# Optimization experiments

Measured on AMD Instinct MI355X. Metric: run time of the kernel, lower is better.

## Reference

```python
import jax, jax.numpy as jnp
import numpy as np
import math

B, T, IN, H, OUT, L = 8, 256, 128, 128, 128, 2
MAX_EP_LEN = 10000.0


def _rotate(x, pos, d):
    # rope as in source: repeat(1,1,2) = concat along last dim (not interleave)
    half = jnp.exp(jnp.arange(0, d, 2, dtype=jnp.float32) * (-math.log(MAX_EP_LEN) / d))  # [d/2]
    ang = pos[..., None] * half  # [B,T,d/2]
    sine = jnp.concatenate([jnp.sin(ang), jnp.sin(ang)], axis=-1)
    cos = jnp.concatenate([jnp.cos(ang), jnp.cos(ang)], axis=-1)
    y1, y2 = jnp.split(x, 2, axis=-1)
    x_rot = jnp.concatenate([-y2, y1], axis=-1)
    return x * cos + x_rot * sine


def _layernorm(x, w, b, eps=1e-5):
    m = jnp.mean(x, axis=-1, keepdims=True)
    v = jnp.mean((x - m) ** 2, axis=-1, keepdims=True)
    return (x - m) / jnp.sqrt(v + eps) * w + b


def _block(x, S0, Z0, Wk, Wq, Wv, lw, lb, w1, b1, w2, b2, scw, scb):
    # x: [B,T,F]; S0: [B,F,F]; Z0: [B,F]
    x = _layernorm(x, lw, lb)
    K = jax.nn.elu(x @ Wk.T) + 1.0
    Q = jax.nn.elu(x @ Wq.T) + 1.0
    V = x @ Wv.T
    outer = jnp.einsum('bti,btj->btij', K, V)  # [B,T,F,F]
    S = jnp.clip(jnp.cumsum(outer, axis=1), -1e20, 1e20) + S0[:, None]  # [B,T,F,F]
    Z = jnp.clip(jnp.cumsum(K, axis=1), -1e20, 1e20) + Z0[:, None]      # [B,T,F]
    num = jnp.einsum('bti,btil->btl', Q, S)
    den = jnp.einsum('bti,bti->bt', Q, Z)[..., None] + 1e-5
    out = num / den
    out = jax.nn.relu(jax.nn.relu(out @ w1.T + b1) @ w2.T + b2)  # feed_forward
    out = out + x @ scw.T + scb                                   # residual shortcut
    return out, S[:, -1], Z[:, -1]


def setup_inputs() -> dict:
    key = jax.random.key(0)
    ks = jax.random.split(key, 14)
    s = 0.05
    return {
        'z': jax.random.normal(ks[0], (T, B, IN), jnp.float32),
        'state': jnp.zeros((B, L * (H * H + H) + 1), jnp.float32),
        'Wk': jax.random.normal(ks[1], (L, H, IN), jnp.float32) * s,
        'Wq': jax.random.normal(ks[2], (L, H, IN), jnp.float32) * s,
        'Wv': jax.random.normal(ks[3], (L, H, IN), jnp.float32) * s,
        'ln_w': jnp.ones((L, IN), jnp.float32),
        'ln_b': jnp.zeros((L, IN), jnp.float32),
        'ff_w1': jax.random.normal(ks[4], (L, H, H), jnp.float32) * s,
        'ff_b1': jnp.zeros((L, H), jnp.float32),
        'ff_w2': jax.random.normal(ks[5], (L, H, H), jnp.float32) * s,
        'ff_b2': jnp.zeros((L, H), jnp.float32),
        'sc_w': jax.random.normal(ks[6], (L, H, IN), jnp.float32) * s,
        'sc_b': jnp.zeros((L, H), jnp.float32),
        'unmap_w': jax.random.normal(ks[7], (OUT, H), jnp.float32) * s,
        'unmap_b': jnp.zeros((OUT,), jnp.float32),
    }


def reference(z, state, Wk, Wq, Wv, ln_w, ln_b, ff_w1, ff_b1, ff_w2, ff_b2, sc_w, sc_b, unmap_w, unmap_b):
    x = jnp.transpose(z, (1, 0, 2))  # [B,T,IN]
    ts = state[:, -1]                # [B] timestep counters
    core = state[:, :-1].reshape(B, L, H * H + H)
    pos = ts[:, None] + jnp.arange(T, dtype=jnp.float32)[None, :]  # [B,T]
    x = _rotate(x, pos, IN)  # embedding_type == 'rope'
    new_states = []
    for i in range(L):
        S0 = core[:, i, :H * H].reshape(B, H, H)
        Z0 = core[:, i, H * H:]
        x, Sl, Zl = _block(x, S0, Z0, Wk[i], Wq[i], Wv[i], ln_w[i], ln_b[i],
                           ff_w1[i], ff_b1[i], ff_w2[i], ff_b2[i], sc_w[i], sc_b[i])
        new_states.append(jnp.concatenate([Sl.reshape(B, -1), Zl], axis=-1))
    y = x @ unmap_w.T + unmap_b
    st = jnp.concatenate([jnp.stack(new_states, axis=1).reshape(B, -1), (ts + T)[:, None]], axis=-1)
    return jnp.transpose(y, (1, 0, 2)), st
```

## Files before the change

kernel.cpp:

```cpp
#include <hip/hip_runtime.h>
#include <math.h>

#define Bn 8
#define Tn 256
#define Hn 128
#define Ln 2
#define COREn (Hn*Hn + Hn)
#define SDn   (Ln*COREn + 1)

typedef __attribute__((ext_vector_type(8))) short short8;
typedef __attribute__((ext_vector_type(4))) short short4v;
typedef __attribute__((ext_vector_type(4))) float floatx4;

#define MFMA16(a,b,c) __builtin_amdgcn_mfma_f32_16x16x32_bf16(a,b,c,0,0,0)

static __device__ __forceinline__ unsigned short f2bf(float f) {
  unsigned int u = __float_as_uint(f);
  return (unsigned short)((u + 0x7FFFu + ((u >> 16) & 1u)) >> 16);
}
static __device__ __forceinline__ float bf2f(unsigned short h) {
  return __uint_as_float((unsigned int)h << 16);
}
static __device__ __forceinline__ short8 ldwfrag(const float* p) {
  float4 a = *(const float4*)p;
  float4 b = *(const float4*)(p + 4);
  short8 r;
  r[0] = (short)f2bf(a.x); r[1] = (short)f2bf(a.y);
  r[2] = (short)f2bf(a.z); r[3] = (short)f2bf(a.w);
  r[4] = (short)f2bf(b.x); r[5] = (short)f2bf(b.y);
  r[6] = (short)f2bf(b.z); r[7] = (short)f2bf(b.w);
  return r;
}
static __device__ __forceinline__ void ld8(const float* p, float* v) {
  float4 a = *(const float4*)p, b = *(const float4*)(p + 4);
  v[0]=a.x; v[1]=a.y; v[2]=a.z; v[3]=a.w; v[4]=b.x; v[5]=b.y; v[6]=b.z; v[7]=b.w;
}

__global__ __launch_bounds__(256) void proj_kernel(
    const float* __restrict__ xsrc, const float* __restrict__ state,
    const float* __restrict__ Wk, const float* __restrict__ Wq,
    const float* __restrict__ Wv, const float* __restrict__ scw,
    const float* __restrict__ lnw, const float* __restrict__ lnb,
    const float* __restrict__ scb,
    unsigned short* __restrict__ Kb, unsigned short* __restrict__ Kt,
    unsigned short* __restrict__ Qb, unsigned short* __restrict__ Vt,
    float* __restrict__ skipb, int is_l0) {
  __shared__ unsigned short xs[16][136];

  const int tid = threadIdx.x;
  const int by  = blockIdx.y;
  const int g0  = blockIdx.x * 16;
  const int r = tid >> 4, c0 = (tid & 15) * 8;
  const int g = g0 + r, b = g >> 8, t = g & 255;

  float v[8];
  if (is_l0) {
    const float* zr = xsrc + ((size_t)t * Bn + b) * 128;
    float pv[8];
    ld8(zr + c0, v);
    ld8(zr + (c0 ^ 64), pv);
    float pos = state[(size_t)b * SDn + SDn - 1] + (float)t;
#pragma unroll
    for (int i = 0; i < 8; i++) {
      int jj = (c0 + i) & 63;
      float ang = pos * expf((float)jj * -0.14391156831212787f);
      float sn = sinf(ang), cs = cosf(ang);
      v[i] = (c0 < 64) ? (v[i] * cs - pv[i] * sn) : (v[i] * cs + pv[i] * sn);
    }
  } else {
    ld8(xsrc + (size_t)g * 128 + c0, v);
  }
  float sm = 0.f, sq = 0.f;
#pragma unroll
  for (int i = 0; i < 8; i++) { sm += v[i]; sq += v[i] * v[i]; }
  for (int d = 8; d; d >>= 1) { sm += __shfl_xor(sm, d, 16); sq += __shfl_xor(sq, d, 16); }
  float mean = sm * (1.f / 128.f);
  float rstd = rsqrtf(sq * (1.f / 128.f) - mean * mean + 1e-5f);
  float lw[8], lb[8];
  ld8(lnw + c0, lw); ld8(lnb + c0, lb);
  short8 xv;
#pragma unroll
  for (int i = 0; i < 8; i++) xv[i] = (short)f2bf((v[i] - mean) * rstd * lw[i] + lb[i]);
  *(short8*)&xs[r][c0] = xv;
  __syncthreads();

  const float* Wsel = (by == 0) ? Wk : (by == 1) ? Wq : (by == 2) ? Wv : scw;
  const int lane = tid & 63, wv = tid >> 6;
  const int lm = lane & 15, quad = lane >> 4;
  floatx4 acc0 = {0.f, 0.f, 0.f, 0.f}, acc1 = {0.f, 0.f, 0.f, 0.f};
#pragma unroll
  for (int kc = 0; kc < 4; kc++) {
    short8 a  = *(const short8*)&xs[lm][kc * 32 + quad * 8];
    short8 b0 = ldwfrag(Wsel + (size_t)(wv * 32 + lm) * 128 + kc * 32 + quad * 8);
    short8 b1 = ldwfrag(Wsel + (size_t)(wv * 32 + 16 + lm) * 128 + kc * 32 + quad * 8);
    acc0 = MFMA16(a, b0, acc0);
    acc1 = MFMA16(a, b1, acc1);
  }
  const int t0l = g0 & 255;
  const int n0 = wv * 32 + lm, n1 = wv * 32 + 16 + lm;
  if (by == 0) {
    short4v kt0, kt1;
#pragma unroll
    for (int j = 0; j < 4; j++) {
      int row = quad * 4 + j;
      float e0 = acc0[j] > 0.f ? acc0[j] + 1.f : expf(acc0[j]);
      float e1 = acc1[j] > 0.f ? acc1[j] + 1.f : expf(acc1[j]);
      Kb[(size_t)(g0 + row) * 128 + n0] = f2bf(e0);
      Kb[(size_t)(g0 + row) * 128 + n1] = f2bf(e1);
      kt0[j] = (short)f2bf(e0); kt1[j] = (short)f2bf(e1);
    }
    *(short4v*)(Kt + (size_t)(b * 128 + n0) * 256 + t0l + quad * 4) = kt0;
    *(short4v*)(Kt + (size_t)(b * 128 + n1) * 256 + t0l + quad * 4) = kt1;
  } else if (by == 1) {
#pragma unroll
    for (int j = 0; j < 4; j++) {
      int row = quad * 4 + j;
      float e0 = acc0[j] > 0.f ? acc0[j] + 1.f : expf(acc0[j]);
      float e1 = acc1[j] > 0.f ? acc1[j] + 1.f : expf(acc1[j]);
      Qb[(size_t)(g0 + row) * 128 + n0] = f2bf(e0);
      Qb[(size_t)(g0 + row) * 128 + n1] = f2bf(e1);
    }
  } else if (by == 2) {
    short4v v0, v1;
#pragma unroll
    for (int j = 0; j < 4; j++) { v0[j] = (short)f2bf(acc0[j]); v1[j] = (short)f2bf(acc1[j]); }
    *(short4v*)(Vt + (size_t)(b * 128 + n0) * 256 + t0l + quad * 4) = v0;
    *(short4v*)(Vt + (size_t)(b * 128 + n1) * 256 + t0l + quad * 4) = v1;
  } else {
    float sb0 = scb[n0], sb1 = scb[n1];
#pragma unroll
    for (int j = 0; j < 4; j++) {
      int row = quad * 4 + j;
      skipb[(size_t)(g0 + row) * 128 + n0] = acc0[j] + sb0;
      skipb[(size_t)(g0 + row) * 128 + n1] = acc1[j] + sb1;
    }
  }
}

__global__ __launch_bounds__(256) void attn_state_kernel(
    const unsigned short* __restrict__ Kb, const unsigned short* __restrict__ Kt,
    const unsigned short* __restrict__ Qb, const unsigned short* __restrict__ Vt,
    const float* __restrict__ state, unsigned short* __restrict__ attnb,
    float* __restrict__ st_out, int l) {
  const int tid = threadIdx.x, bx = blockIdx.x;
  const int lane = tid & 63, wv = tid >> 6, lm = lane & 15, quad = lane >> 4;

  if (bx < 128) {
    __shared__ unsigned short xs[16][136];
    __shared__ unsigned short Ssc[4][16][40];
    __shared__ float Obuf[4][16][132];
    __shared__ float Z0s[128];
    __shared__ float denw[4][16];
    __shared__ float denz[16];
    __shared__ float dinv[16];

    const int b = bx >> 4, rt = bx & 15, t0 = rt * 16;
    const size_t sb = (size_t)b * SDn + (size_t)l * COREn;
    {
      int r = tid >> 4, c = (tid & 15) * 8;
      *(short8*)&xs[r][c] = *(const short8*)(Qb + (size_t)(b * 256 + t0 + r) * 128 + c);
    }
    if (tid < 128) Z0s[tid] = state[sb + 16384 + tid];
    __syncthreads();

    {
      int r = tid >> 4, c = (tid & 15) * 8;
      float qz = 0.f;
#pragma unroll
      for (int i = 0; i < 8; i++) qz += bf2f(xs[r][c + i]) * Z0s[c + i];
      for (int d = 8; d; d >>= 1) qz += __shfl_xor(qz, d, 16);
      if ((tid & 15) == 0) denz[r] = qz;
    }

    floatx4 oacc[8];
#pragma unroll
    for (int jt = 0; jt < 8; jt++) oacc[jt] = floatx4{0.f, 0.f, 0.f, 0.f};
    float dacc[4] = {0.f, 0.f, 0.f, 0.f};

    const int nch = rt / 2 + 1;
    for (int c = wv; c < nch; c += 4) {
      const int kb = c * 32;
      floatx4 s0 = {0.f,0.f,0.f,0.f}, s1 = {0.f,0.f,0.f,0.f};
#pragma unroll
      for (int kc = 0; kc < 4; kc++) {
        short8 a  = *(const short8*)&xs[lm][kc * 32 + quad * 8];
        short8 k0 = *(const short8*)(Kb + (size_t)(b * 256 + kb + lm) * 128 + kc * 32 + quad * 8);
        short8 k1 = *(const short8*)(Kb + (size_t)(b * 256 + kb + 16 + lm) * 128 + kc * 32 + quad * 8);
        s0 = MFMA16(a, k0, s0);
        s1 = MFMA16(a, k1, s1);
      }
      const int tau0 = kb + lm, tau1 = kb + 16 + lm;
#pragma unroll
      for (int j = 0; j < 4; j++) {
        int m = t0 + quad * 4 + j;
        float v0 = (tau0 <= m) ? s0[j] : 0.f;
        float v1 = (tau1 <= m) ? s1[j] : 0.f;
        dacc[j] += v0 + v1;
        Ssc[wv][quad * 4 + j][lm]      = f2bf(v0);
        Ssc[wv][quad * 4 + j][16 + lm] = f2bf(v1);
      }
      short8 sa = *(const short8*)&Ssc[wv][lm][quad * 8];
#pragma unroll
      for (int jt = 0; jt < 8; jt++) {
        short8 vb = *(const short8*)(Vt + (size_t)(b * 128 + jt * 16 + lm) * 256 + kb + quad * 8);
        oacc[jt] = MFMA16(sa, vb, oacc[jt]);
      }
    }

    {
      const float* S0 = state + sb;
      short8 aq = *(const short8*)&xs[lm][wv * 32 + quad * 8];
#pragma unroll
      for (int jt = 0; jt < 8; jt++) {
        short8 vb;
#pragma unroll
        for (int jj = 0; jj < 8; jj++)
          vb[jj] = (short)f2bf(S0[(size_t)(wv * 32 + quad * 8 + jj) * 128 + jt * 16 + lm]);
        oacc[jt] = MFMA16(aq, vb, oacc[jt]);
      }
    }

#pragma unroll
    for (int j = 0; j < 4; j++)
      for (int d = 8; d; d >>= 1) dacc[j] += __shfl_xor(dacc[j], d, 16);
    if (lm == 0) {
#pragma unroll
      for (int j = 0; j < 4; j++) denw[wv][quad * 4 + j] = dacc[j];
    }
#pragma unroll
    for (int jt = 0; jt < 8; jt++)
#pragma unroll
      for (int j = 0; j < 4; j++)
        Obuf[wv][quad * 4 + j][jt * 16 + lm] = oacc[jt][j];
    __syncthreads();
    if (tid < 16) {
      float d = denz[tid] + denw[0][tid] + denw[1][tid] + denw[2][tid] + denw[3][tid] + 1e-5f;
      dinv[tid] = 1.f / d;
    }
    __syncthreads();
    {
      int r = tid >> 4, c = (tid & 15) * 8;
      float di = dinv[r];
      short8 ov;
#pragma unroll
      for (int i = 0; i < 8; i++) {
        float o = Obuf[0][r][c + i] + Obuf[1][r][c + i] + Obuf[2][r][c + i] + Obuf[3][r][c + i];
        ov[i] = (short)f2bf(o * di);
      }
      *(short8*)(attnb + (size_t)(b * 256 + t0 + r) * 128 + c) = ov;
    }
  } else {
    const int idx = bx - 128;
    const int b = idx >> 4, sub = idx & 15;
    const int i0 = (sub >> 1) * 16, j0 = (sub & 1) * 64;
    const size_t sb = (size_t)b * SDn + (size_t)l * COREn;
    floatx4 acc = {0.f, 0.f, 0.f, 0.f};
#pragma unroll
    for (int kc = 0; kc < 8; kc++) {
      short8 ka = *(const short8*)(Kt + (size_t)(b * 128 + i0 + lm) * 256 + kc * 32 + quad * 8);
      short8 vb = *(const short8*)(Vt + (size_t)(b * 128 + j0 + wv * 16 + lm) * 256 + kc * 32 + quad * 8);
      acc = MFMA16(ka, vb, acc);
    }
#pragma unroll
    for (int j = 0; j < 4; j++) {
      size_t off = sb + (size_t)(i0 + quad * 4 + j) * 128 + j0 + wv * 16 + lm;
      st_out[off] = acc[j] + state[off];
    }
    if (j0 == 0) {
      if (tid < 128) {
        int i = tid >> 3, seg = tid & 7;
        const unsigned short* kr = Kt + (size_t)(b * 128 + i0 + i) * 256 + seg * 32;
        float zs = 0.f;
#pragma unroll
        for (int x = 0; x < 4; x++) {
          short8 kv = *(const short8*)(kr + x * 8);
#pragma unroll
          for (int y = 0; y < 8; y++) zs += bf2f((unsigned short)kv[y]);
        }
        for (int d = 4; d; d >>= 1) zs += __shfl_xor(zs, d, 8);
        if (seg == 0) {
          size_t zo = sb + 16384 + i0 + i;
          st_out[zo] = zs + state[zo];
        }
      }
      if (sub == 0 && tid == 0 && l == 0)
        st_out[(size_t)b * SDn + SDn - 1] = state[(size_t)b * SDn + SDn - 1] + 256.f;
    }
  }
}

__global__ __launch_bounds__(256) void ff_kernel(
    const unsigned short* __restrict__ attnb, const float* __restrict__ skipb,
    const float* __restrict__ w1, const float* __restrict__ b1,
    const float* __restrict__ w2, const float* __restrict__ b2,
    const float* __restrict__ unw, const float* __restrict__ unb,
    float* __restrict__ xout, float* __restrict__ yout, int do_unmap) {
  __shared__ unsigned short xs[16][136];
  __shared__ unsigned short hs[16][136];
  __shared__ float sk[16][132];

  const int tid = threadIdx.x;
  const int g0 = blockIdx.x * 16;
  const int lane = tid & 63, wv = tid >> 6, lm = lane & 15, quad = lane >> 4;
  const int n0 = wv * 32 + lm, n1 = wv * 32 + 16 + lm;

  {
    int r = tid >> 4, c = (tid & 15) * 8;
    *(short8*)&xs[r][c] = *(const short8*)(attnb + (size_t)(g0 + r) * 128 + c);
#pragma unroll
    for (int p = 0; p < 2; p++) {
      int f = tid + p * 256;
      int rr = f >> 5, cc = (f & 31) * 4;
      *(float4*)&sk[rr][cc] = *(const float4*)(skipb + (size_t)(g0 + rr) * 128 + cc);
    }
  }
  __syncthreads();

  {
    floatx4 a0 = {0.f,0.f,0.f,0.f}, a1 = {0.f,0.f,0.f,0.f};
#pragma unroll
    for (int kc = 0; kc < 4; kc++) {
      short8 a  = *(const short8*)&xs[lm][kc * 32 + quad * 8];
      short8 bA = ldwfrag(w1 + (size_t)n0 * 128 + kc * 32 + quad * 8);
      short8 bB = ldwfrag(w1 + (size_t)n1 * 128 + kc * 32 + quad * 8);
      a0 = MFMA16(a, bA, a0);
      a1 = MFMA16(a, bB, a1);
    }
    float bi0 = b1[n0], bi1 = b1[n1];
#pragma unroll
    for (int j = 0; j < 4; j++) {
      int row = quad * 4 + j;
      hs[row][n0] = f2bf(fmaxf(a0[j] + bi0, 0.f));
      hs[row][n1] = f2bf(fmaxf(a1[j] + bi1, 0.f));
    }
  }
  __syncthreads();

  float o0[4], o1[4];
  {
    floatx4 a0 = {0.f,0.f,0.f,0.f}, a1 = {0.f,0.f,0.f,0.f};
#pragma unroll
    for (int kc = 0; kc < 4; kc++) {
      short8 a  = *(const short8*)&hs[lm][kc * 32 + quad * 8];
      short8 bA = ldwfrag(w2 + (size_t)n0 * 128 + kc * 32 + quad * 8);
      short8 bB = ldwfrag(w2 + (size_t)n1 * 128 + kc * 32 + quad * 8);
      a0 = MFMA16(a, bA, a0);
      a1 = MFMA16(a, bB, a1);
    }
    float bi0 = b2[n0], bi1 = b2[n1];
#pragma unroll
    for (int j = 0; j < 4; j++) {
      int row = quad * 4 + j;
      o0[j] = fmaxf(a0[j] + bi0, 0.f) + sk[row][n0];
      o1[j] = fmaxf(a1[j] + bi1, 0.f) + sk[row][n1];
    }
  }
  if (!do_unmap) {
#pragma unroll
    for (int j = 0; j < 4; j++) {
      int row = quad * 4 + j;
      xout[(size_t)(g0 + row) * 128 + n0] = o0[j];
      xout[(size_t)(g0 + row) * 128 + n1] = o1[j];
    }
    return;
  }
  __syncthreads();
#pragma unroll
  for (int j = 0; j < 4; j++) {
    int row = quad * 4 + j;
    xs[row][n0] = f2bf(o0[j]);
    xs[row][n1] = f2bf(o1[j]);
  }
  __syncthreads();
  {
    floatx4 a0 = {0.f,0.f,0.f,0.f}, a1 = {0.f,0.f,0.f,0.f};
#pragma unroll
    for (int kc = 0; kc < 4; kc++) {
      short8 a  = *(const short8*)&xs[lm][kc * 32 + quad * 8];
      short8 bA = ldwfrag(unw + (size_t)n0 * 128 + kc * 32 + quad * 8);
      short8 bB = ldwfrag(unw + (size_t)n1 * 128 + kc * 32 + quad * 8);
      a0 = MFMA16(a, bA, a0);
      a1 = MFMA16(a, bB, a1);
    }
    float u0 = unb[n0], u1 = unb[n1];
#pragma unroll
    for (int j = 0; j < 4; j++) {
      int gg = g0 + quad * 4 + j;
      int bb = gg >> 8, tq = gg & 255;
      yout[(size_t)(tq * Bn + bb) * 128 + n0] = a0[j] + u0;
      yout[(size_t)(tq * Bn + bb) * 128 + n1] = a1[j] + u1;
    }
  }
}

extern "C" void kernel_launch(void* const* d_in, const int* in_sizes, int n_in,
                              void* d_out, int out_size, void* d_ws, size_t ws_size,
                              hipStream_t stream) {
  const float* z       = (const float*)d_in[0];
  const float* state   = (const float*)d_in[1];
  const float* Wk      = (const float*)d_in[2];
  const float* Wq      = (const float*)d_in[3];
  const float* Wv      = (const float*)d_in[4];
  const float* ln_w    = (const float*)d_in[5];
  const float* ln_b    = (const float*)d_in[6];
  const float* ff_w1   = (const float*)d_in[7];
  const float* ff_b1   = (const float*)d_in[8];
  const float* ff_w2   = (const float*)d_in[9];
  const float* ff_b2   = (const float*)d_in[10];
  const float* sc_w    = (const float*)d_in[11];
  const float* sc_b    = (const float*)d_in[12];
  const float* unmap_w = (const float*)d_in[13];
  const float* unmap_b = (const float*)d_in[14];

  float* y_out  = (float*)d_out;
  float* st_out = y_out + (size_t)Tn * Bn * 128;

  const size_t E = 262144;
  unsigned short* Kb    = (unsigned short*)d_ws;
  unsigned short* Qb    = Kb + E;
  unsigned short* Kt    = Qb + E;
  unsigned short* Vt    = Kt + E;
  unsigned short* attnb = Vt + E;
  float* skipb = (float*)(attnb + E);
  float* xbuf  = skipb + E;

  for (int l = 0; l < Ln; l++) {
    proj_kernel<<<dim3(128, 4), 256, 0, stream>>>(
        (l == 0) ? z : xbuf, state,
        Wk + (size_t)l * 16384, Wq + (size_t)l * 16384,
        Wv + (size_t)l * 16384, sc_w + (size_t)l * 16384,
        ln_w + (size_t)l * 128, ln_b + (size_t)l * 128, sc_b + (size_t)l * 128,
        Kb, Kt, Qb, Vt, skipb, (l == 0) ? 1 : 0);

    attn_state_kernel<<<256, 256, 0, stream>>>(
        Kb, Kt, Qb, Vt, state, attnb, st_out, l);

    ff_kernel<<<128, 256, 0, stream>>>(
        attnb, skipb,
        ff_w1 + (size_t)l * 16384, ff_b1 + (size_t)l * 128,
        ff_w2 + (size_t)l * 16384, ff_b2 + (size_t)l * 128,
        unmap_w, unmap_b, xbuf, y_out, (l == 1) ? 1 : 0);
  }
}
```

Baseline: 138.2 us.

## Fuse attention, feed-forward and next-layer projection into per-layer kernels

Replaces the six-launch sequence (projection, attention/state, feed-forward for each layer) with three launches. Attention output now stays in shared memory and feeds the feed-forward directly, and layer 0's feed-forward epilogue computes layernorm plus the layer-1 K/Q/V/skip projections in place. Separate workspace buffers per layer avoid overwriting inputs still being read. Fewer launches and fewer intermediate global round trips, at the cost of more shared memory per block and fewer projection blocks running in parallel.

Result: no change. 135.6 us (-1.8%).

```diff
diff --git a/kernel.cpp b/kernel.cpp
--- a/kernel.cpp
+++ b/kernel.cpp
@@ -3,10 +3,8 @@
 
 #define Bn 8
 #define Tn 256
-#define Hn 128
-#define Ln 2
-#define COREn (Hn*Hn + Hn)
-#define SDn   (Ln*COREn + 1)
+#define COREn 16512
+#define SDn   33025
 
 typedef __attribute__((ext_vector_type(8))) short short8;
 typedef __attribute__((ext_vector_type(4))) short short4v;
@@ -36,68 +34,31 @@
   v[0]=a.x; v[1]=a.y; v[2]=a.z; v[3]=a.w; v[4]=b.x; v[5]=b.y; v[6]=b.z; v[7]=b.w;
 }
 
-__global__ __launch_bounds__(256) void proj_kernel(
-    const float* __restrict__ xsrc, const float* __restrict__ state,
-    const float* __restrict__ Wk, const float* __restrict__ Wq,
-    const float* __restrict__ Wv, const float* __restrict__ scw,
-    const float* __restrict__ lnw, const float* __restrict__ lnb,
-    const float* __restrict__ scb,
+struct Phase1 {
+  unsigned short Ssc[4][16][40];
+  float Obuf[4][16][132];
+  float denw[4][16];
+};
+struct Phase2 {
+  float sk[16][132];
+  float os[16][132];
+};
+struct Smem {
+  unsigned short xs[16][136];
+  unsigned short xattn[16][136];
+  unsigned short hs[16][136];
+  float Z0s[128];
+  float denz[16];
+  float dinv[16];
+  union { Phase1 p1; Phase2 p2; } u;
+};
+
+static __device__ __forceinline__ void proj_epilogue(
+    int by, int g0, int b, int t0l, int n0, int n1, int quad,
+    floatx4 acc0, floatx4 acc1,
     unsigned short* __restrict__ Kb, unsigned short* __restrict__ Kt,
     unsigned short* __restrict__ Qb, unsigned short* __restrict__ Vt,
-    float* __restrict__ skipb, int is_l0) {
-  __shared__ unsigned short xs[16][136];
-
-  const int tid = threadIdx.x;
-  const int by  = blockIdx.y;
-  const int g0  = blockIdx.x * 16;
-  const int r = tid >> 4, c0 = (tid & 15) * 8;
-  const int g = g0 + r, b = g >> 8, t = g & 255;
-
-  float v[8];
-  if (is_l0) {
-    const float* zr = xsrc + ((size_t)t * Bn + b) * 128;
-    float pv[8];
-    ld8(zr + c0, v);
-    ld8(zr + (c0 ^ 64), pv);
-    float pos = state[(size_t)b * SDn + SDn - 1] + (float)t;
-#pragma unroll
-    for (int i = 0; i < 8; i++) {
-      int jj = (c0 + i) & 63;
-      float ang = pos * expf((float)jj * -0.14391156831212787f);
-      float sn = sinf(ang), cs = cosf(ang);
-      v[i] = (c0 < 64) ? (v[i] * cs - pv[i] * sn) : (v[i] * cs + pv[i] * sn);
-    }
-  } else {
-    ld8(xsrc + (size_t)g * 128 + c0, v);
-  }
-  float sm = 0.f, sq = 0.f;
-#pragma unroll
-  for (int i = 0; i < 8; i++) { sm += v[i]; sq += v[i] * v[i]; }
-  for (int d = 8; d; d >>= 1) { sm += __shfl_xor(sm, d, 16); sq += __shfl_xor(sq, d, 16); }
-  float mean = sm * (1.f / 128.f);
-  float rstd = rsqrtf(sq * (1.f / 128.f) - mean * mean + 1e-5f);
-  float lw[8], lb[8];
-  ld8(lnw + c0, lw); ld8(lnb + c0, lb);
-  short8 xv;
-#pragma unroll
-  for (int i = 0; i < 8; i++) xv[i] = (short)f2bf((v[i] - mean) * rstd * lw[i] + lb[i]);
-  *(short8*)&xs[r][c0] = xv;
-  __syncthreads();
-
-  const float* Wsel = (by == 0) ? Wk : (by == 1) ? Wq : (by == 2) ? Wv : scw;
-  const int lane = tid & 63, wv = tid >> 6;
-  const int lm = lane & 15, quad = lane >> 4;
-  floatx4 acc0 = {0.f, 0.f, 0.f, 0.f}, acc1 = {0.f, 0.f, 0.f, 0.f};
-#pragma unroll
-  for (int kc = 0; kc < 4; kc++) {
-    short8 a  = *(const short8*)&xs[lm][kc * 32 + quad * 8];
-    short8 b0 = ldwfrag(Wsel + (size_t)(wv * 32 + lm) * 128 + kc * 32 + quad * 8);
-    short8 b1 = ldwfrag(Wsel + (size_t)(wv * 32 + 16 + lm) * 128 + kc * 32 + quad * 8);
-    acc0 = MFMA16(a, b0, acc0);
-    acc1 = MFMA16(a, b1, acc1);
-  }
-  const int t0l = g0 & 255;
-  const int n0 = wv * 32 + lm, n1 = wv * 32 + 16 + lm;
+    float* __restrict__ skipb, const float* __restrict__ scb) {
   if (by == 0) {
     short4v kt0, kt1;
 #pragma unroll
@@ -137,190 +98,126 @@
   }
 }
 
-__global__ __launch_bounds__(256) void attn_state_kernel(
-    const unsigned short* __restrict__ Kb, const unsigned short* __restrict__ Kt,
-    const unsigned short* __restrict__ Qb, const unsigned short* __restrict__ Vt,
-    const float* __restrict__ state, unsigned short* __restrict__ attnb,
-    float* __restrict__ st_out, int l) {
-  const int tid = threadIdx.x, bx = blockIdx.x;
-  const int lane = tid & 63, wv = tid >> 6, lm = lane & 15, quad = lane >> 4;
-
-  if (bx < 128) {
-    __shared__ unsigned short xs[16][136];
-    __shared__ unsigned short Ssc[4][16][40];
-    __shared__ float Obuf[4][16][132];
-    __shared__ float Z0s[128];
-    __shared__ float denw[4][16];
-    __shared__ float denz[16];
-    __shared__ float dinv[16];
-
-    const int b = bx >> 4, rt = bx & 15, t0 = rt * 16;
-    const size_t sb = (size_t)b * SDn + (size_t)l * COREn;
-    {
-      int r = tid >> 4, c = (tid & 15) * 8;
-      *(short8*)&xs[r][c] = *(const short8*)(Qb + (size_t)(b * 256 + t0 + r) * 128 + c);
-    }
-    if (tid < 128) Z0s[tid] = state[sb + 16384 + tid];
-    __syncthreads();
-
-    {
-      int r = tid >> 4, c = (tid & 15) * 8;
-      float qz = 0.f;
-#pragma unroll
-      for (int i = 0; i < 8; i++) qz += bf2f(xs[r][c + i]) * Z0s[c + i];
-      for (int d = 8; d; d >>= 1) qz += __shfl_xor(qz, d, 16);
-      if ((tid & 15) == 0) denz[r] = qz;
-    }
-
-    floatx4 oacc[8];
-#pragma unroll
-    for (int jt = 0; jt < 8; jt++) oacc[jt] = floatx4{0.f, 0.f, 0.f, 0.f};
-    float dacc[4] = {0.f, 0.f, 0.f, 0.f};
-
-    const int nch = rt / 2 + 1;
-    for (int c = wv; c < nch; c += 4) {
-      const int kb = c * 32;
-      floatx4 s0 = {0.f,0.f,0.f,0.f}, s1 = {0.f,0.f,0.f,0.f};
-#pragma unroll
-      for (int kc = 0; kc < 4; kc++) {
-        short8 a  = *(const short8*)&xs[lm][kc * 32 + quad * 8];
-        short8 k0 = *(const short8*)(Kb + (size_t)(b * 256 + kb + lm) * 128 + kc * 32 + quad * 8);
-        short8 k1 = *(const short8*)(Kb + (size_t)(b * 256 + kb + 16 + lm) * 128 + kc * 32 + quad * 8);
-        s0 = MFMA16(a, k0, s0);
-        s1 = MFMA16(a, k1, s1);
-      }
-      const int tau0 = kb + lm, tau1 = kb + 16 + lm;
-#pragma unroll
-      for (int j = 0; j < 4; j++) {
-        int m = t0 + quad * 4 + j;
-        float v0 = (tau0 <= m) ? s0[j] : 0.f;
-        float v1 = (tau1 <= m) ? s1[j] : 0.f;
-        dacc[j] += v0 + v1;
-        Ssc[wv][quad * 4 + j][lm]      = f2bf(v0);
-        Ssc[wv][quad * 4 + j][16 + lm] = f2bf(v1);
-      }
-      short8 sa = *(const short8*)&Ssc[wv][lm][quad * 8];
-#pragma unroll
-      for (int jt = 0; jt < 8; jt++) {
-        short8 vb = *(const short8*)(Vt + (size_t)(b * 128 + jt * 16 + lm) * 256 + kb + quad * 8);
-        oacc[jt] = MFMA16(sa, vb, oacc[jt]);
-      }
-    }
-
-    {
-      const float* S0 = state + sb;
-      short8 aq = *(const short8*)&xs[lm][wv * 32 + quad * 8];
-#pragma unroll
-      for (int jt = 0; jt < 8; jt++) {
-        short8 vb;
-#pragma unroll
-        for (int jj = 0; jj < 8; jj++)
-          vb[jj] = (short)f2bf(S0[(size_t)(wv * 32 + quad * 8 + jj) * 128 + jt * 16 + lm]);
-        oacc[jt] = MFMA16(aq, vb, oacc[jt]);
-      }
-    }
-
-#pragma unroll
-    for (int j = 0; j < 4; j++)
-      for (int d = 8; d; d >>= 1) dacc[j] += __shfl_xor(dacc[j], d, 16);
-    if (lm == 0) {
-#pragma unroll
-      for (int j = 0; j < 4; j++) denw[wv][quad * 4 + j] = dacc[j];
-    }
-#pragma unroll
-    for (int jt = 0; jt < 8; jt++)
-#pragma unroll
-      for (int j = 0; j < 4; j++)
-        Obuf[wv][quad * 4 + j][jt * 16 + lm] = oacc[jt][j];
-    __syncthreads();
-    if (tid < 16) {
-      float d = denz[tid] + denw[0][tid] + denw[1][tid] + denw[2][tid] + denw[3][tid] + 1e-5f;
-      dinv[tid] = 1.f / d;
-    }
-    __syncthreads();
-    {
-      int r = tid >> 4, c = (tid & 15) * 8;
-      float di = dinv[r];
-      short8 ov;
-#pragma unroll
-      for (int i = 0; i < 8; i++) {
-        float o = Obuf[0][r][c + i] + Obuf[1][r][c + i] + Obuf[2][r][c + i] + Obuf[3][r][c + i];
-        ov[i] = (short)f2bf(o * di);
-      }
-      *(short8*)(attnb + (size_t)(b * 256 + t0 + r) * 128 + c) = ov;
-    }
-  } else {
-    const int idx = bx - 128;
-    const int b = idx >> 4, sub = idx & 15;
-    const int i0 = (sub >> 1) * 16, j0 = (sub & 1) * 64;
-    const size_t sb = (size_t)b * SDn + (size_t)l * COREn;
-    floatx4 acc = {0.f, 0.f, 0.f, 0.f};
-#pragma unroll
-    for (int kc = 0; kc < 8; kc++) {
-      short8 ka = *(const short8*)(Kt + (size_t)(b * 128 + i0 + lm) * 256 + kc * 32 + quad * 8);
-      short8 vb = *(const short8*)(Vt + (size_t)(b * 128 + j0 + wv * 16 + lm) * 256 + kc * 32 + quad * 8);
-      acc = MFMA16(ka, vb, acc);
-    }
-#pragma unroll
-    for (int j = 0; j < 4; j++) {
-      size_t off = sb + (size_t)(i0 + quad * 4 + j) * 128 + j0 + wv * 16 + lm;
-      st_out[off] = acc[j] + state[off];
-    }
-    if (j0 == 0) {
-      if (tid < 128) {
-        int i = tid >> 3, seg = tid & 7;
-        const unsigned short* kr = Kt + (size_t)(b * 128 + i0 + i) * 256 + seg * 32;
-        float zs = 0.f;
-#pragma unroll
-        for (int x = 0; x < 4; x++) {
-          short8 kv = *(const short8*)(kr + x * 8);
-#pragma unroll
-          for (int y = 0; y < 8; y++) zs += bf2f((unsigned short)kv[y]);
-        }
-        for (int d = 4; d; d >>= 1) zs += __shfl_xor(zs, d, 8);
-        if (seg == 0) {
-          size_t zo = sb + 16384 + i0 + i;
-          st_out[zo] = zs + state[zo];
-        }
-      }
-      if (sub == 0 && tid == 0 && l == 0)
-        st_out[(size_t)b * SDn + SDn - 1] = state[(size_t)b * SDn + SDn - 1] + 256.f;
-    }
-  }
-}
-
-__global__ __launch_bounds__(256) void ff_kernel(
-    const unsigned short* __restrict__ attnb, const float* __restrict__ skipb,
+static __device__ void attn_ff(
+    Smem& s, int tid, int b, int rt, int l,
+    const unsigned short* __restrict__ Kb, const unsigned short* __restrict__ Qb,
+    const unsigned short* __restrict__ Vt,
+    const float* __restrict__ state, const float* __restrict__ skipin,
     const float* __restrict__ w1, const float* __restrict__ b1,
     const float* __restrict__ w2, const float* __restrict__ b2,
+    const float* __restrict__ Wk1, const float* __restrict__ Wq1,
+    const float* __restrict__ Wv1, const float* __restrict__ scw1,
+    const float* __restrict__ lnw1, const float* __restrict__ lnb1,
+    const float* __restrict__ scb1,
+    unsigned short* __restrict__ Kb1, unsigned short* __restrict__ Kt1,
+    unsigned short* __restrict__ Qb1, unsigned short* __restrict__ Vt1,
+    float* __restrict__ skip1,
     const float* __restrict__ unw, const float* __restrict__ unb,
-    float* __restrict__ xout, float* __restrict__ yout, int do_unmap) {
-  __shared__ unsigned short xs[16][136];
-  __shared__ unsigned short hs[16][136];
-  __shared__ float sk[16][132];
-
-  const int tid = threadIdx.x;
-  const int g0 = blockIdx.x * 16;
+    float* __restrict__ yout) {
   const int lane = tid & 63, wv = tid >> 6, lm = lane & 15, quad = lane >> 4;
-  const int n0 = wv * 32 + lm, n1 = wv * 32 + 16 + lm;
-
-  {
-    int r = tid >> 4, c = (tid & 15) * 8;
-    *(short8*)&xs[r][c] = *(const short8*)(attnb + (size_t)(g0 + r) * 128 + c);
-#pragma unroll
-    for (int p = 0; p < 2; p++) {
-      int f = tid + p * 256;
-      int rr = f >> 5, cc = (f & 31) * 4;
-      *(float4*)&sk[rr][cc] = *(const float4*)(skipb + (size_t)(g0 + rr) * 128 + cc);
-    }
-  }
+  const int t0 = rt * 16;
+  const size_t sb = (size_t)b * SDn + (size_t)l * COREn;
+
+  { int r = tid >> 4, c = (tid & 15) * 8;
+    *(short8*)&s.xs[r][c] = *(const short8*)(Qb + (size_t)(b * 256 + t0 + r) * 128 + c); }
+  if (tid < 128) s.Z0s[tid] = state[sb + 16384 + tid];
   __syncthreads();
 
-  {
-    floatx4 a0 = {0.f,0.f,0.f,0.f}, a1 = {0.f,0.f,0.f,0.f};
+  { int r = tid >> 4, c = (tid & 15) * 8;
+    float qz = 0.f;
+#pragma unroll
+    for (int i = 0; i < 8; i++) qz += bf2f(s.xs[r][c + i]) * s.Z0s[c + i];
+    for (int d = 8; d; d >>= 1) qz += __shfl_xor(qz, d, 16);
+    if ((tid & 15) == 0) s.denz[r] = qz; }
+
+  floatx4 oacc[8];
+#pragma unroll
+  for (int jt = 0; jt < 8; jt++) oacc[jt] = floatx4{0.f, 0.f, 0.f, 0.f};
+  float dacc[4] = {0.f, 0.f, 0.f, 0.f};
+
+  const int nch = rt / 2 + 1;
+  for (int c = wv; c < nch; c += 4) {
+    const int kb = c * 32;
+    floatx4 s0 = {0.f,0.f,0.f,0.f}, s1 = {0.f,0.f,0.f,0.f};
 #pragma unroll
     for (int kc = 0; kc < 4; kc++) {
-      short8 a  = *(const short8*)&xs[lm][kc * 32 + quad * 8];
+      short8 a  = *(const short8*)&s.xs[lm][kc * 32 + quad * 8];
+      short8 k0 = *(const short8*)(Kb + (size_t)(b * 256 + kb + lm) * 128 + kc * 32 + quad * 8);
+      short8 k1 = *(const short8*)(Kb + (size_t)(b * 256 + kb + 16 + lm) * 128 + kc * 32 + quad * 8);
+      s0 = MFMA16(a, k0, s0);
+      s1 = MFMA16(a, k1, s1);
+    }
+    const int tau0 = kb + lm, tau1 = kb + 16 + lm;
+#pragma unroll
+    for (int j = 0; j < 4; j++) {
+      int m = t0 + quad * 4 + j;
+      float v0 = (tau0 <= m) ? s0[j] : 0.f;
+      float v1 = (tau1 <= m) ? s1[j] : 0.f;
+      dacc[j] += v0 + v1;
+      s.u.p1.Ssc[wv][quad * 4 + j][lm]      = f2bf(v0);
+      s.u.p1.Ssc[wv][quad * 4 + j][16 + lm] = f2bf(v1);
+    }
+    short8 sa = *(const short8*)&s.u.p1.Ssc[wv][lm][quad * 8];
+#pragma unroll
+    for (int jt = 0; jt < 8; jt++) {
+      short8 vb = *(const short8*)(Vt + (size_t)(b * 128 + jt * 16 + lm) * 256 + kb + quad * 8);
+      oacc[jt] = MFMA16(sa, vb, oacc[jt]);
+    }
+  }
+
+  { const float* S0 = state + sb;
+    short8 aq = *(const short8*)&s.xs[lm][wv * 32 + quad * 8];
+#pragma unroll
+    for (int jt = 0; jt < 8; jt++) {
+      short8 vb;
+#pragma unroll
+      for (int jj = 0; jj < 8; jj++)
+        vb[jj] = (short)f2bf(S0[(size_t)(wv * 32 + quad * 8 + jj) * 128 + jt * 16 + lm]);
+      oacc[jt] = MFMA16(aq, vb, oacc[jt]);
+    } }
+
+#pragma unroll
+  for (int j = 0; j < 4; j++)
+    for (int d = 8; d; d >>= 1) dacc[j] += __shfl_xor(dacc[j], d, 16);
+  if (lm == 0) {
+#pragma unroll
+    for (int j = 0; j < 4; j++) s.u.p1.denw[wv][quad * 4 + j] = dacc[j];
+  }
+#pragma unroll
+  for (int jt = 0; jt < 8; jt++)
+#pragma unroll
+    for (int j = 0; j < 4; j++)
+      s.u.p1.Obuf[wv][quad * 4 + j][jt * 16 + lm] = oacc[jt][j];
+  __syncthreads();
+  if (tid < 16)
+    s.dinv[tid] = 1.f / (s.denz[tid] + s.u.p1.denw[0][tid] + s.u.p1.denw[1][tid]
+                         + s.u.p1.denw[2][tid] + s.u.p1.denw[3][tid] + 1e-5f);
+  __syncthreads();
+  { int r = tid >> 4, c = (tid & 15) * 8;
+    float di = s.dinv[r];
+    short8 ov;
+#pragma unroll
+    for (int i = 0; i < 8; i++) {
+      float o = s.u.p1.Obuf[0][r][c + i] + s.u.p1.Obuf[1][r][c + i]
+              + s.u.p1.Obuf[2][r][c + i] + s.u.p1.Obuf[3][r][c + i];
+      ov[i] = (short)f2bf(o * di);
+    }
+    *(short8*)&s.xattn[r][c] = ov; }
+  __syncthreads();
+
+  const int gr0 = b * 256 + t0;
+#pragma unroll
+  for (int p = 0; p < 2; p++) {
+    int f = tid + p * 256;
+    int rr = f >> 5, cc = (f & 31) * 4;
+    *(float4*)&s.u.p2.sk[rr][cc] = *(const float4*)(skipin + (size_t)(gr0 + rr) * 128 + cc);
+  }
+  const int n0 = wv * 32 + lm, n1 = n0 + 16;
+
+  { floatx4 a0 = {0.f,0.f,0.f,0.f}, a1 = {0.f,0.f,0.f,0.f};
+#pragma unroll
+    for (int kc = 0; kc < 4; kc++) {
+      short8 a  = *(const short8*)&s.xattn[lm][kc * 32 + quad * 8];
       short8 bA = ldwfrag(w1 + (size_t)n0 * 128 + kc * 32 + quad * 8);
       short8 bB = ldwfrag(w1 + (size_t)n1 * 128 + kc * 32 + quad * 8);
       a0 = MFMA16(a, bA, a0);
@@ -330,18 +227,16 @@
 #pragma unroll
     for (int j = 0; j < 4; j++) {
       int row = quad * 4 + j;
-      hs[row][n0] = f2bf(fmaxf(a0[j] + bi0, 0.f));
-      hs[row][n1] = f2bf(fmaxf(a1[j] + bi1, 0.f));
-    }
-  }
+      s.hs[row][n0] = f2bf(fmaxf(a0[j] + bi0, 0.f));
+      s.hs[row][n1] = f2bf(fmaxf(a1[j] + bi1, 0.f));
+    } }
   __syncthreads();
 
   float o0[4], o1[4];
-  {
-    floatx4 a0 = {0.f,0.f,0.f,0.f}, a1 = {0.f,0.f,0.f,0.f};
+  { floatx4 a0 = {0.f,0.f,0.f,0.f}, a1 = {0.f,0.f,0.f,0.f};
 #pragma unroll
     for (int kc = 0; kc < 4; kc++) {
-      short8 a  = *(const short8*)&hs[lm][kc * 32 + quad * 8];
+      short8 a  = *(const short8*)&s.hs[lm][kc * 32 + quad * 8];
       short8 bA = ldwfrag(w2 + (size_t)n0 * 128 + kc * 32 + quad * 8);
       short8 bB = ldwfrag(w2 + (size_t)n1 * 128 + kc * 32 + quad * 8);
       a0 = MFMA16(a, bA, a0);
@@ -351,32 +246,61 @@
 #pragma unroll
     for (int j = 0; j < 4; j++) {
       int row = quad * 4 + j;
-      o0[j] = fmaxf(a0[j] + bi0, 0.f) + sk[row][n0];
-      o1[j] = fmaxf(a1[j] + bi1, 0.f) + sk[row][n1];
-    }
-  }
-  if (!do_unmap) {
-#pragma unroll
-    for (int j = 0; j < 4; j++) {
-      int row = quad * 4 + j;
-      xout[(size_t)(g0 + row) * 128 + n0] = o0[j];
-      xout[(size_t)(g0 + row) * 128 + n1] = o1[j];
-    }
-    return;
-  }
-  __syncthreads();
-#pragma unroll
-  for (int j = 0; j < 4; j++) {
-    int row = quad * 4 + j;
-    xs[row][n0] = f2bf(o0[j]);
-    xs[row][n1] = f2bf(o1[j]);
-  }
-  __syncthreads();
-  {
+      o0[j] = fmaxf(a0[j] + bi0, 0.f) + s.u.p2.sk[row][n0];
+      o1[j] = fmaxf(a1[j] + bi1, 0.f) + s.u.p2.sk[row][n1];
+    } }
+
+  if (l == 0) {
+#pragma unroll
+    for (int j = 0; j < 4; j++) {
+      int row = quad * 4 + j;
+      s.u.p2.os[row][n0] = o0[j];
+      s.u.p2.os[row][n1] = o1[j];
+    }
+    __syncthreads();
+    { int r = tid >> 4, c0 = (tid & 15) * 8;
+      float v[8];
+#pragma unroll
+      for (int i = 0; i < 8; i++) v[i] = s.u.p2.os[r][c0 + i];
+      float sm = 0.f, sq = 0.f;
+#pragma unroll
+      for (int i = 0; i < 8; i++) { sm += v[i]; sq += v[i] * v[i]; }
+      for (int d = 8; d; d >>= 1) { sm += __shfl_xor(sm, d, 16); sq += __shfl_xor(sq, d, 16); }
+      float mean = sm * (1.f / 128.f);
+      float rstd = rsqrtf(sq * (1.f / 128.f) - mean * mean + 1e-5f);
+      short8 xv;
+#pragma unroll
+      for (int i = 0; i < 8; i++)
+        xv[i] = (short)f2bf((v[i] - mean) * rstd * lnw1[c0 + i] + lnb1[c0 + i]);
+      *(short8*)&s.xs[r][c0] = xv; }
+    __syncthreads();
+#pragma unroll
+    for (int by = 0; by < 4; by++) {
+      const float* W = by == 0 ? Wk1 : by == 1 ? Wq1 : by == 2 ? Wv1 : scw1;
+      floatx4 a0 = {0.f,0.f,0.f,0.f}, a1 = {0.f,0.f,0.f,0.f};
+#pragma unroll
+      for (int kc = 0; kc < 4; kc++) {
+        short8 a  = *(const short8*)&s.xs[lm][kc * 32 + quad * 8];
+        short8 bA = ldwfrag(W + (size_t)n0 * 128 + kc * 32 + quad * 8);
+        short8 bB = ldwfrag(W + (size_t)n1 * 128 + kc * 32 + quad * 8);
+        a0 = MFMA16(a, bA, a0);
+        a1 = MFMA16(a, bB, a1);
+      }
+      proj_epilogue(by, gr0, b, t0, n0, n1, quad, a0, a1,
+                    Kb1, Kt1, Qb1, Vt1, skip1, scb1);
+    }
+  } else {
+#pragma unroll
+    for (int j = 0; j < 4; j++) {
+      int row = quad * 4 + j;
+      s.xs[row][n0] = f2bf(o0[j]);
+      s.xs[row][n1] = f2bf(o1[j]);
+    }
+    __syncthreads();
     floatx4 a0 = {0.f,0.f,0.f,0.f}, a1 = {0.f,0.f,0.f,0.f};
 #pragma unroll
     for (int kc = 0; kc < 4; kc++) {
-      short8 a  = *(const short8*)&xs[lm][kc * 32 + quad * 8];
+      short8 a  = *(const short8*)&s.xs[lm][kc * 32 + quad * 8];
       short8 bA = ldwfrag(unw + (size_t)n0 * 128 + kc * 32 + quad * 8);
       short8 bB = ldwfrag(unw + (size_t)n1 * 128 + kc * 32 + quad * 8);
       a0 = MFMA16(a, bA, a0);
@@ -385,12 +309,162 @@
     float u0 = unb[n0], u1 = unb[n1];
 #pragma unroll
     for (int j = 0; j < 4; j++) {
-      int gg = g0 + quad * 4 + j;
+      int gg = gr0 + quad * 4 + j;
       int bb = gg >> 8, tq = gg & 255;
       yout[(size_t)(tq * Bn + bb) * 128 + n0] = a0[j] + u0;
       yout[(size_t)(tq * Bn + bb) * 128 + n1] = a1[j] + u1;
     }
   }
+}
+
+static __device__ void state_upd(
+    int tid, int idx, int l,
+    const unsigned short* __restrict__ Kt, const unsigned short* __restrict__ Vt,
+    const float* __restrict__ state, float* __restrict__ st_out) {
+  const int lane = tid & 63, wv = tid >> 6, lm = lane & 15, quad = lane >> 4;
+  const int b = idx >> 4, sub = idx & 15;
+  const int i0 = (sub >> 1) * 16, j0 = (sub & 1) * 64;
+  const size_t sb = (size_t)b * SDn + (size_t)l * COREn;
+  floatx4 acc = {0.f, 0.f, 0.f, 0.f};
+#pragma unroll
+  for (int kc = 0; kc < 8; kc++) {
+    short8 ka = *(const short8*)(Kt + (size_t)(b * 128 + i0 + lm) * 256 + kc * 32 + quad * 8);
+    short8 vb = *(const short8*)(Vt + (size_t)(b * 128 + j0 + wv * 16 + lm) * 256 + kc * 32 + quad * 8);
+    acc = MFMA16(ka, vb, acc);
+  }
+#pragma unroll
+  for (int j = 0; j < 4; j++) {
+    size_t off = sb + (size_t)(i0 + quad * 4 + j) * 128 + j0 + wv * 16 + lm;
+    st_out[off] = acc[j] + state[off];
+  }
+  if (j0 == 0) {
+    if (tid < 128) {
+      int i = tid >> 3, seg = tid & 7;
+      const unsigned short* kr = Kt + (size_t)(b * 128 + i0 + i) * 256 + seg * 32;
+      float zs = 0.f;
+#pragma unroll
+      for (int x = 0; x < 4; x++) {
+        short8 kv = *(const short8*)(kr + x * 8);
+#pragma unroll
+        for (int y = 0; y < 8; y++) zs += bf2f((unsigned short)kv[y]);
+      }
+      for (int d = 4; d; d >>= 1) zs += __shfl_xor(zs, d, 8);
+      if (seg == 0) {
+        size_t zo = sb + 16384 + i0 + i;
+        st_out[zo] = zs + state[zo];
+      }
+    }
+    if (sub == 0 && tid == 0 && l == 0)
+      st_out[(size_t)b * SDn + SDn - 1] = state[(size_t)b * SDn + SDn - 1] + 256.f;
+  }
+}
+
+__global__ __launch_bounds__(256) void proj0_kernel(
+    const float* __restrict__ z, const float* __restrict__ state,
+    const float* __restrict__ Wk, const float* __restrict__ Wq,
+    const float* __restrict__ Wv, const float* __restrict__ scw,
+    const float* __restrict__ lnw, const float* __restrict__ lnb,
+    const float* __restrict__ scb,
+    unsigned short* __restrict__ Kb0, unsigned short* __restrict__ Qb0,
+    unsigned short* __restrict__ Kt0, unsigned short* __restrict__ Vt0,
+    float* __restrict__ skip0) {
+  __shared__ unsigned short xs[16][136];
+  const int tid = threadIdx.x, bx = blockIdx.x;
+  const int lane = tid & 63, wv = tid >> 6, lm = lane & 15, quad = lane >> 4;
+  const int tile = bx >> 1, half = bx & 1;
+  const int g0 = tile * 16;
+  const int r = tid >> 4, c0 = (tid & 15) * 8;
+  const int g = g0 + r, b = g >> 8, t = g & 255;
+  float v[8], pv[8];
+  const float* zr = z + ((size_t)t * Bn + b) * 128;
+  ld8(zr + c0, v);
+  ld8(zr + (c0 ^ 64), pv);
+  float pos = state[(size_t)b * SDn + SDn - 1] + (float)t;
+#pragma unroll
+  for (int i = 0; i < 8; i++) {
+    int jj = (c0 + i) & 63;
+    float ang = pos * expf((float)jj * -0.14391156831212787f);
+    float sn = sinf(ang), cs = cosf(ang);
+    v[i] = (c0 < 64) ? (v[i] * cs - pv[i] * sn) : (v[i] * cs + pv[i] * sn);
+  }
+  float sm = 0.f, sq = 0.f;
+#pragma unroll
+  for (int i = 0; i < 8; i++) { sm += v[i]; sq += v[i] * v[i]; }
+  for (int d = 8; d; d >>= 1) { sm += __shfl_xor(sm, d, 16); sq += __shfl_xor(sq, d, 16); }
+  float mean = sm * (1.f / 128.f);
+  float rstd = rsqrtf(sq * (1.f / 128.f) - mean * mean + 1e-5f);
+  short8 xv;
+#pragma unroll
+  for (int i = 0; i < 8; i++)
+    xv[i] = (short)f2bf((v[i] - mean) * rstd * lnw[c0 + i] + lnb[c0 + i]);
+  *(short8*)&xs[r][c0] = xv;
+  __syncthreads();
+
+  const int bb = g0 >> 8, t0l = g0 & 255;
+  const int n0 = wv * 32 + lm, n1 = n0 + 16;
+#pragma unroll
+  for (int which = 0; which < 2; which++) {
+    const float* W = half == 0 ? (which == 0 ? Wk : Wq)
+                               : (which == 0 ? Wv : scw);
+    floatx4 a0 = {0.f,0.f,0.f,0.f}, a1 = {0.f,0.f,0.f,0.f};
+#pragma unroll
+    for (int kc = 0; kc < 4; kc++) {
+      short8 a  = *(const short8*)&xs[lm][kc * 32 + quad * 8];
+      short8 bA = ldwfrag(W + (size_t)n0 * 128 + kc * 32 + quad * 8);
+      short8 bB = ldwfrag(W + (size_t)n1 * 128 + kc * 32 + quad * 8);
+      a0 = MFMA16(a, bA, a0);
+      a1 = MFMA16(a, bB, a1);
+    }
+    proj_epilogue(half * 2 + which, g0, bb, t0l, n0, n1, quad, a0, a1,
+                  Kb0, Kt0, Qb0, Vt0, skip0, scb);
+  }
+}
+
+__global__ __launch_bounds__(256) void layer0_kernel(
+    const unsigned short* __restrict__ Kb0, const unsigned short* __restrict__ Qb0,
+    const unsigned short* __restrict__ Kt0, const unsigned short* __restrict__ Vt0,
+    const float* __restrict__ skip0, const float* __restrict__ state,
+    const float* __restrict__ w1, const float* __restrict__ b1,
+    const float* __restrict__ w2, const float* __restrict__ b2,
+    const float* __restrict__ Wk1, const float* __restrict__ Wq1,
+    const float* __restrict__ Wv1, const float* __restrict__ scw1,
+    const float* __restrict__ lnw1, const float* __restrict__ lnb1,
+    const float* __restrict__ scb1,
+    unsigned short* __restrict__ Kb1, unsigned short* __restrict__ Kt1,
+    unsigned short* __restrict__ Qb1, unsigned short* __restrict__ Vt1,
+    float* __restrict__ skip1, float* __restrict__ st_out) {
+  __shared__ Smem s;
+  const int tid = threadIdx.x, bx = blockIdx.x;
+  if (bx < 128)
+    attn_ff(s, tid, bx >> 4, bx & 15, 0,
+            Kb0, Qb0, Vt0, state, skip0,
+            w1, b1, w2, b2,
+            Wk1, Wq1, Wv1, scw1, lnw1, lnb1, scb1,
+            Kb1, Kt1, Qb1, Vt1, skip1,
+            nullptr, nullptr, nullptr);
+  else
+    state_upd(tid, bx - 128, 0, Kt0, Vt0, state, st_out);
+}
+
+__global__ __launch_bounds__(256) void layer1_kernel(
+    const unsigned short* __restrict__ Kb1, const unsigned short* __restrict__ Qb1,
+    const unsigned short* __restrict__ Kt1, const unsigned short* __restrict__ Vt1,
+    const float* __restrict__ skip1, const float* __restrict__ state,
+    const float* __restrict__ w1, const float* __restrict__ b1,
+    const float* __restrict__ w2, const float* __restrict__ b2,
+    const float* __restrict__ unw, const float* __restrict__ unb,
+    float* __restrict__ yout, float* __restrict__ st_out) {
+  __shared__ Smem s;
+  const int tid = threadIdx.x, bx = blockIdx.x;
+  if (bx < 128)
+    attn_ff(s, tid, bx >> 4, bx & 15, 1,
+            Kb1, Qb1, Vt1, state, skip1,
+            w1, b1, w2, b2,
+            nullptr, nullptr, nullptr, nullptr, nullptr, nullptr, nullptr,
+            nullptr, nullptr, nullptr, nullptr, nullptr,
+            unw, unb, yout);
+  else
+    state_upd(tid, bx - 128, 1, Kt1, Vt1, state, st_out);
 }
 
 extern "C" void kernel_launch(void* const* d_in, const int* in_sizes, int n_in,
@@ -416,29 +490,30 @@
   float* st_out = y_out + (size_t)Tn * Bn * 128;
 
   const size_t E = 262144;
-  unsigned short* Kb    = (unsigned short*)d_ws;
-  unsigned short* Qb    = Kb + E;
-  unsigned short* Kt    = Qb + E;
-  unsigned short* Vt    = Kt + E;
-  unsigned short* attnb = Vt + E;
-  float* skipb = (float*)(attnb + E);
-  float* xbuf  = skipb + E;
-
-  for (int l = 0; l < Ln; l++) {
-    proj_kernel<<<dim3(128, 4), 256, 0, stream>>>(
-        (l == 0) ? z : xbuf, state,
-        Wk + (size_t)l * 16384, Wq + (size_t)l * 16384,
-        Wv + (size_t)l * 16384, sc_w + (size_t)l * 16384,
-        ln_w + (size_t)l * 128, ln_b + (size_t)l * 128, sc_b + (size_t)l * 128,
-        Kb, Kt, Qb, Vt, skipb, (l == 0) ? 1 : 0);
-
-    attn_state_kernel<<<256, 256, 0, stream>>>(
-        Kb, Kt, Qb, Vt, state, attnb, st_out, l);
-
-    ff_kernel<<<128, 256, 0, stream>>>(
-        attnb, skipb,
-        ff_w1 + (size_t)l * 16384, ff_b1 + (size_t)l * 128,
-        ff_w2 + (size_t)l * 16384, ff_b2 + (size_t)l * 128,
-        unmap_w, unmap_b, xbuf, y_out, (l == 1) ? 1 : 0);
-  }
-}
+  unsigned short* Kb0 = (unsigned short*)d_ws;
+  unsigned short* Qb0 = Kb0 + E;
+  unsigned short* Kt0 = Qb0 + E;
+  unsigned short* Vt0 = Kt0 + E;
+  unsigned short* Kb1 = Vt0 + E;
+  unsigned short* Qb1 = Kb1 + E;
+  unsigned short* Kt1 = Qb1 + E;
+  unsigned short* Vt1 = Kt1 + E;
+  float* skip0 = (float*)(Vt1 + E);
+  float* skip1 = skip0 + E;
+
+  proj0_kernel<<<256, 256, 0, stream>>>(
+      z, state, Wk, Wq, Wv, sc_w, ln_w, ln_b, sc_b,
+      Kb0, Qb0, Kt0, Vt0, skip0);
+
+  layer0_kernel<<<256, 256, 0, stream>>>(
+      Kb0, Qb0, Kt0, Vt0, skip0, state,
+      ff_w1, ff_b1, ff_w2, ff_b2,
+      Wk + 16384, Wq + 16384, Wv + 16384, sc_w + 16384,
+      ln_w + 128, ln_b + 128, sc_b + 128,
+      Kb1, Kt1, Qb1, Vt1, skip1, st_out);
+
+  layer1_kernel<<<256, 256, 0, stream>>>(
+      Kb1, Qb1, Kt1, Vt1, skip1, state,
+      ff_w1 + 16384, ff_b1 + 128, ff_w2 + 16384, ff_b2 + 128,
+      unmap_w, unmap_b, y_out, st_out);
+}
```
